# Optimization experiments

Hardware: AMD Instinct MI355X
Metric: run time of the kernel (lower is better)

Reference implementation:

```python
import jax, jax.numpy as jnp
import numpy as np

WINDOW_SIZE = 11
VAL_RANGE = 1.0
N_CHANNEL = 3
MS_WEIGHTS = jnp.array([0.0448, 0.2856, 0.3001, 0.2363, 0.1333], dtype=jnp.float32)


def _gaussian_window(window_size, sigma, channel):
    x = jnp.arange(window_size, dtype=jnp.float32)
    g = jnp.exp(-((x - window_size // 2) ** 2) / (2.0 * sigma ** 2))
    g = g / jnp.sum(g)
    w2d = jnp.outer(g, g)  # [ws, ws]
    # depthwise kernel in OIHW with feature_group_count=channel: [C, 1, ws, ws]
    return jnp.broadcast_to(w2d[None, None], (channel, 1, window_size, window_size))


def _dwconv(x, kernel):
    # x: [B, C, H, W], kernel: [C, 1, ws, ws], valid padding, groups=C
    return jax.lax.conv_general_dilated(
        x, kernel, window_strides=(1, 1), padding='VALID',
        dimension_numbers=('NCHW', 'OIHW', 'NCHW'),
        feature_group_count=kernel.shape[0])


def _avg_pool2(x):
    # kernel 2, stride 2, no padding (floor mode)
    s = jax.lax.reduce_window(x, 0.0, jax.lax.add,
                              (1, 1, 2, 2), (1, 1, 2, 2), 'VALID')
    return s * 0.25


def setup_inputs() -> dict:
    key = jax.random.key(0)
    k1, k2 = jax.random.split(key)
    output = jax.random.uniform(k1, (16, 3, 512, 512), dtype=jnp.float32)
    target = jax.random.uniform(k2, (16, 3, 512, 512), dtype=jnp.float32)
    return {"output": output, "target": target}


def reference(output, target):
    window = _gaussian_window(WINDOW_SIZE, 1.5, N_CHANNEL)
    L = VAL_RANGE
    C1 = (0.01 * L) ** 2
    C2 = (0.03 * L) ** 2
    cs_list, ssim_list = [], []
    for _ in range(MS_WEIGHTS.shape[0]):
        mu1 = _dwconv(output, window)
        mu2 = _dwconv(target, window)
        sigma1_sq = _dwconv(output * output, window) - mu1 * mu1
        sigma2_sq = _dwconv(target * target, window) - mu2 * mu2
        sigma12 = _dwconv(output * target, window) - mu1 * mu2
        denom = sigma1_sq + sigma2_sq + C2
        cs = (2.0 * sigma12 + C2) / denom
        ssim = (2.0 * mu1 * mu2 + C1) * (2.0 * sigma12 + C2) / (
            (mu1 * mu1 + mu2 * mu2 + C1) * denom)
        cs_list.append(jax.nn.relu(jnp.mean(cs)))
        ssim_list.append(jax.nn.relu(jnp.mean(ssim)))
        output = _avg_pool2(output)
        target = _avg_pool2(target)
    cs = (jnp.stack(cs_list) + 1.0) / 2.0
    ssim = (jnp.stack(ssim_list) + 1.0) / 2.0
    ms_ssim = jnp.prod((cs ** MS_WEIGHTS)[:-1]) * (ssim ** MS_WEIGHTS)[-1]
    return 1.0 - ms_ssim
```

## Files before the change

kernel.cpp:

```cpp
#include <hip/hip_runtime.h>

#define HALO 10
#define NIMG 48

#define GWLIST { 0.0010284f, 0.0075987f, 0.0360008f, 0.1093607f, 0.2130056f, \
                 0.2660117f, 0.2130056f, 0.1093607f, 0.0360008f, 0.0075987f, 0.0010284f }

#define PP   48
#define PSZ  (48 * 48)
#define HT0  (5 * PSZ)
#define HTP  48
#define HTSZ (32 * 48)
#define LDSH (HT0 + 5 * HTSZ)

typedef _Float16 half8 __attribute__((ext_vector_type(8)));
typedef _Float16 half4 __attribute__((ext_vector_type(4)));
typedef float    floatx4 __attribute__((ext_vector_type(4)));

template <bool FUSE>
__global__ __launch_bounds__(256, 4) void ssim_mfma_kernel(
    const float* __restrict__ A, const float* __restrict__ B,
    int H, int W, float2* __restrict__ partial,
    float* __restrict__ poolA, float* __restrict__ poolB)
{
    __shared__ __align__(16) _Float16 sm[LDSH];
    __shared__ float red[16];

    const float w[11] = GWLIST;
    const int tid  = threadIdx.x;
    const int lane = tid & 63;
    const int wv   = tid >> 6;
    const int gx0  = blockIdx.x * 32;
    const int gy0  = blockIdx.y * 32;
    const int z    = blockIdx.z;
    const float* a = A + (size_t)z * H * W;
    const float* b = B + (size_t)z * H * W;

    half8 wfrag;
    {
        int base = ((lane >> 4) << 3) - (lane & 15);
        #pragma unroll
        for (int i = 0; i < 8; ++i) {
            int j = base + i;
            float v = 0.f;
            #pragma unroll
            for (int J = 0; J < 11; ++J) v = (j == J) ? w[J] : v;
            wfrag[i] = (_Float16)v;
        }
    }

    const bool fast = (gy0 + 48 <= H) && (gx0 + 48 <= W);
    for (int e = tid; e < 288; e += 256) {
        int r = e / 6, c8 = e - r * 6;
        float fa[8], fb[8];
        if (fast) {
            const float* pa = a + (size_t)(gy0 + r) * W + gx0 + c8 * 8;
            const float* pb = b + (size_t)(gy0 + r) * W + gx0 + c8 * 8;
            *(float4*)&fa[0] = *(const float4*)pa;
            *(float4*)&fa[4] = *(const float4*)(pa + 4);
            *(float4*)&fb[0] = *(const float4*)pb;
            *(float4*)&fb[4] = *(const float4*)(pb + 4);
        } else {
            int gy = gy0 + r;
            #pragma unroll
            for (int i = 0; i < 8; ++i) {
                int gx = gx0 + c8 * 8 + i;
                bool ok = (gy < H) && (gx < W);
                size_t idx = (size_t)gy * W + gx;
                fa[i] = ok ? a[idx] : 0.f;
                fb[i] = ok ? b[idx] : 0.f;
            }
        }
        half8 ha, hb, haa, hbb, hab;
        #pragma unroll
        for (int i = 0; i < 8; ++i) {
            ha[i] = (_Float16)fa[i];
            hb[i] = (_Float16)fb[i];
            float qa = (float)ha[i];
            float qb = (float)hb[i];
            haa[i] = (_Float16)(qa * qa);
            hbb[i] = (_Float16)(qb * qb);
            hab[i] = (_Float16)(qa * qb);
        }
        int o = r * PP + c8 * 8;
        *(half8*)&sm[o + 0 * PSZ] = ha;
        *(half8*)&sm[o + 1 * PSZ] = hb;
        *(half8*)&sm[o + 2 * PSZ] = haa;
        *(half8*)&sm[o + 3 * PSZ] = hbb;
        *(half8*)&sm[o + 4 * PSZ] = hab;
    }
    __syncthreads();

    {
        const int arow = (lane & 15) * PP + ((lane >> 4) << 3);
        const int crow = (lane & 15) * HTP + ((lane >> 4) << 2);
        for (int jj = wv; jj < 30; jj += 4) {
            int q = jj / 6, rem = jj - q * 6;
            int m0 = (rem >> 1) << 4;
            int x0 = (rem & 1) << 4;
            half8 afrag = *(const half8*)&sm[q * PSZ + m0 * PP + x0 + arow];
            floatx4 c = {0.f, 0.f, 0.f, 0.f};
            c = __builtin_amdgcn_mfma_f32_16x16x32_f16(afrag, wfrag, c, 0, 0, 0);
            half4 hv;
            hv[0] = (_Float16)c[0]; hv[1] = (_Float16)c[1];
            hv[2] = (_Float16)c[2]; hv[3] = (_Float16)c[3];
            *(half4*)&sm[HT0 + q * HTSZ + x0 * HTP + m0 + crow] = hv;
        }
    }
    __syncthreads();

    float csSum = 0.f, ssimSum = 0.f;
    {
        const int y0 = (wv >> 1) << 4;
        const int x0 = (wv & 1) << 4;
        const int brow = (lane & 15) * HTP + ((lane >> 4) << 3);
        floatx4 m[5];
        #pragma unroll
        for (int q = 0; q < 5; ++q) {
            half8 bfrag = *(const half8*)&sm[HT0 + q * HTSZ + x0 * HTP + y0 + brow];
            floatx4 c = {0.f, 0.f, 0.f, 0.f};
            m[q] = __builtin_amdgcn_mfma_f32_16x16x32_f16(wfrag, bfrag, c, 0, 0, 0);
        }
        const int OH = H - HALO, OW = W - HALO;
        const int gx  = gx0 + x0 + (lane & 15);
        const int gyb = gy0 + y0 + ((lane >> 4) << 2);
        const float C1 = 1e-4f;
        const float C2 = 9e-4f;
        if (gx < OW) {
            #pragma unroll
            for (int i = 0; i < 4; ++i) {
                int gy = gyb + i;
                if (gy < OH) {
                    float mu1 = m[0][i], mu2 = m[1][i];
                    float s1sq = m[2][i] - mu1 * mu1;
                    float s2sq = m[3][i] - mu2 * mu2;
                    float s12  = m[4][i] - mu1 * mu2;
                    float denom = s1sq + s2sq + C2;
                    float num   = 2.f * s12 + C2;
                    float csv = num * __frcp_rn(denom);
                    float ssv = csv * (2.f * mu1 * mu2 + C1) *
                                __frcp_rn(mu1 * mu1 + mu2 * mu2 + C1);
                    csSum   += csv;
                    ssimSum += ssv;
                }
            }
        }
    }

    #pragma unroll
    for (int off = 32; off > 0; off >>= 1) {
        csSum   += __shfl_down(csSum, off, 64);
        ssimSum += __shfl_down(ssimSum, off, 64);
    }
    if (lane == 0) {
        red[wv]     = csSum;
        red[8 + wv] = ssimSum;
    }
    __syncthreads();
    if (tid == 0) {
        float c = 0.f, s = 0.f;
        #pragma unroll
        for (int i = 0; i < 4; ++i) { c += red[i]; s += red[8 + i]; }
        int slot = (z * gridDim.y + blockIdx.y) * gridDim.x + blockIdx.x;
        partial[slot] = make_float2(c, s);
    }

    if (FUSE && tid < 128) {
        const int OH2 = H >> 1, OW2 = W >> 1;
        const int img = tid >> 6;
        const int rem = tid & 63;
        const int pr  = rem >> 2;
        const int pq  = rem & 3;
        const float* src = img ? b : a;
        float* dst = (img ? poolB : poolA) + (size_t)z * OH2 * OW2;
        size_t base = (size_t)(gy0 + 2 * pr) * W + gx0 + pq * 8;
        float4 r0 = *(const float4*)(src + base);
        float4 r1 = *(const float4*)(src + base + 4);
        float4 r2 = *(const float4*)(src + base + W);
        float4 r3 = *(const float4*)(src + base + W + 4);
        float4 o;
        o.x = 0.25f * (r0.x + r0.y + r2.x + r2.y);
        o.y = 0.25f * (r0.z + r0.w + r2.z + r2.w);
        o.z = 0.25f * (r1.x + r1.y + r3.x + r3.y);
        o.w = 0.25f * (r1.z + r1.w + r3.z + r3.w);
        *(float4*)(dst + (size_t)((gy0 >> 1) + pr) * OW2 + (gx0 >> 1) + pq * 4) = o;
    }
}

#define TH   32
#define ROWS (TH + HALO)
#define HSTR 32
#define HQ   (ROWS * HSTR)

template <bool FUSE>
__global__ __launch_bounds__(256, 5) void ssim_scalar_kernel(
    const float* __restrict__ A, const float* __restrict__ B,
    int H, int W, float2* __restrict__ partial,
    float* __restrict__ poolA, float* __restrict__ poolB)
{
    __shared__ __align__(16) float lds[5 * HQ];
    __shared__ float red[16];

    const float w[11] = GWLIST;

    const int tid = threadIdx.x;
    const int gx0 = blockIdx.x * 32;
    const int gy0 = blockIdx.y * TH;
    const int z   = blockIdx.z;
    const float* a = A + (size_t)z * H * W;
    const float* b = B + (size_t)z * H * W;

    const bool fast = (gy0 + ROWS <= H) && (gx0 + 44 <= W);
    for (int e = tid; e < ROWS * 8; e += 256) {
        int r = e >> 3, c0 = (e & 7) * 4;
        int gy = gy0 + r;
        float s1[4]  = {0.f, 0.f, 0.f, 0.f};
        float s2[4]  = {0.f, 0.f, 0.f, 0.f};
        float s11[4] = {0.f, 0.f, 0.f, 0.f};
        float s22[4] = {0.f, 0.f, 0.f, 0.f};
        float s12[4] = {0.f, 0.f, 0.f, 0.f};
        #pragma unroll
        for (int c = 0; c < 4; ++c) {
            float ea[4], eb[4];
            if (fast) {
                const float* pa = a + (size_t)gy * W + gx0 + c0 + 4 * c;
                const float* pb = b + (size_t)gy * W + gx0 + c0 + 4 * c;
                *(float4*)&ea[0] = *(const float4*)pa;
                *(float4*)&eb[0] = *(const float4*)pb;
            } else {
                #pragma unroll
                for (int t = 0; t < 4; ++t) {
                    int gx = gx0 + c0 + 4 * c + t;
                    bool ok = (gy < H) && (gx < W);
                    size_t idx = (size_t)gy * W + gx;
                    ea[t] = ok ? a[idx] : 0.f;
                    eb[t] = ok ? b[idx] : 0.f;
                }
            }
            #pragma unroll
            for (int mm = 0; mm < 4; ++mm) {
                const int i = 4 * c + mm;
                float va = ea[mm], vb = eb[mm];
                float vaa = va * va, vbb = vb * vb, vab = va * vb;
                #pragma unroll
                for (int k = 0; k < 4; ++k) {
                    const int j = i - k;
                    if (j >= 0 && j <= 10) {
                        float wj = w[j];
                        s1[k]  += wj * va;
                        s2[k]  += wj * vb;
                        s11[k] += wj * vaa;
                        s22[k] += wj * vbb;
                        s12[k] += wj * vab;
                    }
                }
            }
        }
        int hb = r * HSTR + c0;
        *(float4*)&lds[hb + 0 * HQ] = make_float4(s1[0],  s1[1],  s1[2],  s1[3]);
        *(float4*)&lds[hb + 1 * HQ] = make_float4(s2[0],  s2[1],  s2[2],  s2[3]);
        *(float4*)&lds[hb + 2 * HQ] = make_float4(s11[0], s11[1], s11[2], s11[3]);
        *(float4*)&lds[hb + 3 * HQ] = make_float4(s22[0], s22[1], s22[2], s22[3]);
        *(float4*)&lds[hb + 4 * HQ] = make_float4(s12[0], s12[1], s12[2], s12[3]);
    }
    __syncthreads();

    const float C1 = 1e-4f;
    const float C2 = 9e-4f;
    float csSum = 0.f, ssimSum = 0.f;
    {
        const int ox  = tid & 31;
        const int oy0 = (tid >> 5) * 4;
        float m[5][4];
        #pragma unroll
        for (int q = 0; q < 5; ++q) {
            const float* hq = &lds[q * HQ + oy0 * HSTR + ox];
            float win[14];
            #pragma unroll
            for (int i = 0; i < 14; ++i) win[i] = hq[i * HSTR];
            #pragma unroll
            for (int k = 0; k < 4; ++k) {
                float acc = 0.f;
                #pragma unroll
                for (int j = 0; j < 11; ++j) acc += w[j] * win[k + j];
                m[q][k] = acc;
            }
        }
        const int OH = H - HALO, OW = W - HALO;
        const int gx = gx0 + ox;
        #pragma unroll
        for (int k = 0; k < 4; ++k) {
            int gy = gy0 + oy0 + k;
            if (gy < OH && gx < OW) {
                float mu1 = m[0][k], mu2 = m[1][k];
                float s1sq = m[2][k] - mu1 * mu1;
                float s2sq = m[3][k] - mu2 * mu2;
                float s12  = m[4][k] - mu1 * mu2;
                float denom  = s1sq + s2sq + C2;
                float num_cs = 2.f * s12 + C2;
                float csv = num_cs * __frcp_rn(denom);
                float ssv = csv * (2.f * mu1 * mu2 + C1) *
                            __frcp_rn(mu1 * mu1 + mu2 * mu2 + C1);
                csSum   += csv;
                ssimSum += ssv;
            }
        }
    }

    #pragma unroll
    for (int off = 32; off > 0; off >>= 1) {
        csSum   += __shfl_down(csSum, off, 64);
        ssimSum += __shfl_down(ssimSum, off, 64);
    }
    int wave = tid >> 6, lane = tid & 63;
    if (lane == 0) {
        red[wave]     = csSum;
        red[8 + wave] = ssimSum;
    }
    __syncthreads();
    if (tid == 0) {
        float c = 0.f, s = 0.f;
        #pragma unroll
        for (int i = 0; i < 4; ++i) { c += red[i]; s += red[8 + i]; }
        int slot = (z * gridDim.y + blockIdx.y) * gridDim.x + blockIdx.x;
        partial[slot] = make_float2(c, s);
    }

    if (FUSE && tid < 128) {
        const int OH2 = H >> 1, OW2 = W >> 1;
        const int img = tid >> 6;
        const int rem = tid & 63;
        const int pr  = rem >> 2;
        const int pq  = rem & 3;
        const float* src = img ? b : a;
        float* dst = (img ? poolB : poolA) + (size_t)z * OH2 * OW2;
        size_t base = (size_t)(gy0 + 2 * pr) * W + gx0 + pq * 8;
        float4 r0 = *(const float4*)(src + base);
        float4 r1 = *(const float4*)(src + base + 4);
        float4 r2 = *(const float4*)(src + base + W);
        float4 r3 = *(const float4*)(src + base + W + 4);
        float4 o;
        o.x = 0.25f * (r0.x + r0.y + r2.x + r2.y);
        o.y = 0.25f * (r0.z + r0.w + r2.z + r2.w);
        o.z = 0.25f * (r1.x + r1.y + r3.x + r3.y);
        o.w = 0.25f * (r1.z + r1.w + r3.z + r3.w);
        *(float4*)(dst + (size_t)((gy0 >> 1) + pr) * OW2 + (gx0 >> 1) + pq * 4) = o;
    }
}

__global__ void final_kernel(const float2* __restrict__ partial, float* __restrict__ out) {
    __shared__ double red[8];
    __shared__ double resC[5], resS[5];
    const int segs[6] = {0, 12288, 15360, 16128, 16320, 16368};
    const int tid = threadIdx.x;
    for (int s = 0; s < 5; ++s) {
        double c = 0.0, v = 0.0;
        for (int i = segs[s] + tid; i < segs[s + 1]; i += 256) {
            float2 p = partial[i];
            c += (double)p.x;
            v += (double)p.y;
        }
        #pragma unroll
        for (int off = 32; off > 0; off >>= 1) {
            c += __shfl_down(c, off, 64);
            v += __shfl_down(v, off, 64);
        }
        int wave = tid >> 6, lane = tid & 63;
        __syncthreads();
        if (lane == 0) { red[wave] = c; red[4 + wave] = v; }
        __syncthreads();
        if (tid == 0) {
            resC[s] = red[0] + red[1] + red[2] + red[3];
            resS[s] = red[4] + red[5] + red[6] + red[7];
        }
    }
    __syncthreads();
    if (tid == 0) {
        const double wgt[5] = {0.0448, 0.2856, 0.3001, 0.2363, 0.1333};
        double ms = 1.0;
        for (int s = 0; s < 5; ++s) {
            int Hs = 512 >> s;
            double cnt = (double)NIMG * (double)(Hs - 10) * (double)(Hs - 10);
            double cs = resC[s] / cnt;
            double sv = resS[s] / cnt;
            if (cs < 0.0) cs = 0.0;
            if (sv < 0.0) sv = 0.0;
            cs = (cs + 1.0) * 0.5;
            sv = (sv + 1.0) * 0.5;
            ms *= pow((s < 4) ? cs : sv, wgt[s]);
        }
        out[0] = (float)(1.0 - ms);
    }
}

extern "C" void kernel_launch(void* const* d_in, const int* in_sizes, int n_in,
                              void* d_out, int out_size, void* d_ws, size_t ws_size,
                              hipStream_t stream) {
    (void)in_sizes; (void)n_in; (void)out_size; (void)ws_size;
    const float* A0 = (const float*)d_in[0];
    const float* B0 = (const float*)d_in[1];
    float* out = (float*)d_out;

    char* ws = (char*)d_ws;
    float2* partial = (float2*)ws;
    float* pyr = (float*)(ws + (1 << 18));

    float* pa[5] = {nullptr, nullptr, nullptr, nullptr, nullptr};
    float* pb[5] = {nullptr, nullptr, nullptr, nullptr, nullptr};
    size_t off = 0;
    for (int s = 1; s <= 4; ++s) {
        int Hs = 512 >> s;
        size_t n = (size_t)NIMG * Hs * Hs;
        pa[s] = pyr + off; off += n;
        pb[s] = pyr + off; off += n;
    }

    const int segs[5] = {0, 12288, 15360, 16128, 16320};

    const float* curA = A0;
    const float* curB = B0;
    for (int s = 0; s < 5; ++s) {
        int Hs = 512 >> s;
        int g  = Hs >> 5;
        dim3 grid(g, g, NIMG);
        if (s < 2) {
            ssim_mfma_kernel<true><<<grid, 256, 0, stream>>>(
                curA, curB, Hs, Hs, partial + segs[s], pa[s + 1], pb[s + 1]);
            curA = pa[s + 1];
            curB = pb[s + 1];
        } else if (s < 4) {
            ssim_scalar_kernel<true><<<grid, 256, 0, stream>>>(
                curA, curB, Hs, Hs, partial + segs[s], pa[s + 1], pb[s + 1]);
            curA = pa[s + 1];
            curB = pb[s + 1];
        } else {
            ssim_scalar_kernel<false><<<grid, 256, 0, stream>>>(
                curA, curB, Hs, Hs, partial + segs[s], nullptr, nullptr);
        }
    }

    final_kernel<<<1, 256, 0, stream>>>(partial, out);
}
```

Measured before the change: 242.8 us.

## Alias horizontal-pass buffer onto input tiles, pad LDS rows, raise occupancy

The horizontal-pass results are now held in registers and written back into the same LDS region that held the input planes, behind an extra barrier. This removes the separate horizontal-transpose buffer and shrinks shared memory so that launch bounds can ask for 5 blocks per CU. Row pitch is padded from 48 to 56 halves to reduce LDS bank conflicts. The weight fragment is built once by the first wave and read from LDS, the products are computed as packed half vectors, and the final reduction loop is unrolled. The costs are an extra barrier, more register pressure from holding the results, and a different fp16 rounding for the squared terms.

```diff
diff --git a/kernel.cpp b/kernel.cpp
--- a/kernel.cpp
+++ b/kernel.cpp
@@ -6,19 +6,19 @@
 #define GWLIST { 0.0010284f, 0.0075987f, 0.0360008f, 0.1093607f, 0.2130056f, \
                  0.2660117f, 0.2130056f, 0.1093607f, 0.0360008f, 0.0075987f, 0.0010284f }
 
-#define PP   48
-#define PSZ  (48 * 48)
-#define HT0  (5 * PSZ)
-#define HTP  48
-#define HTSZ (32 * 48)
-#define LDSH (HT0 + 5 * HTSZ)
+#define PP   56
+#define PSZ  (48 * 56)
+#define HTP  56
+#define HTSZ (32 * 56)
+#define WT0  (5 * PSZ)
+#define LDSH (WT0 + 64 * 8)
 
 typedef _Float16 half8 __attribute__((ext_vector_type(8)));
 typedef _Float16 half4 __attribute__((ext_vector_type(4)));
 typedef float    floatx4 __attribute__((ext_vector_type(4)));
 
 template <bool FUSE>
-__global__ __launch_bounds__(256, 4) void ssim_mfma_kernel(
+__global__ __launch_bounds__(256, 5) void ssim_mfma_kernel(
     const float* __restrict__ A, const float* __restrict__ B,
     int H, int W, float2* __restrict__ partial,
     float* __restrict__ poolA, float* __restrict__ poolB)
@@ -36,17 +36,18 @@
     const float* a = A + (size_t)z * H * W;
     const float* b = B + (size_t)z * H * W;
 
-    half8 wfrag;
-    {
-        int base = ((lane >> 4) << 3) - (lane & 15);
+    if (tid < 64) {
+        int base = ((tid >> 4) << 3) - (tid & 15);
+        half8 wf;
         #pragma unroll
         for (int i = 0; i < 8; ++i) {
             int j = base + i;
             float v = 0.f;
             #pragma unroll
             for (int J = 0; J < 11; ++J) v = (j == J) ? w[J] : v;
-            wfrag[i] = (_Float16)v;
-        }
+            wf[i] = (_Float16)v;
+        }
+        *(half8*)&sm[WT0 + tid * 8] = wf;
     }
 
     const bool fast = (gy0 + 48 <= H) && (gx0 + 48 <= W);
@@ -71,17 +72,15 @@
                 fb[i] = ok ? b[idx] : 0.f;
             }
         }
-        half8 ha, hb, haa, hbb, hab;
+        half8 ha, hb;
         #pragma unroll
         for (int i = 0; i < 8; ++i) {
             ha[i] = (_Float16)fa[i];
             hb[i] = (_Float16)fb[i];
-            float qa = (float)ha[i];
-            float qb = (float)hb[i];
-            haa[i] = (_Float16)(qa * qa);
-            hbb[i] = (_Float16)(qb * qb);
-            hab[i] = (_Float16)(qa * qb);
-        }
+        }
+        half8 haa = ha * ha;
+        half8 hbb = hb * hb;
+        half8 hab = ha * hb;
         int o = r * PP + c8 * 8;
         *(half8*)&sm[o + 0 * PSZ] = ha;
         *(half8*)&sm[o + 1 * PSZ] = hb;
@@ -91,20 +90,41 @@
     }
     __syncthreads();
 
+    const half8 wfrag = *(const half8*)&sm[WT0 + lane * 8];
+
+    half4 res[8];
     {
         const int arow = (lane & 15) * PP + ((lane >> 4) << 3);
+        #pragma unroll
+        for (int u = 0; u < 8; ++u) {
+            int jj = wv + 4 * u;
+            if (jj < 30) {
+                int q = jj / 6, rem = jj - q * 6;
+                int m0 = (rem >> 1) << 4;
+                int x0 = (rem & 1) << 4;
+                half8 afrag = *(const half8*)&sm[q * PSZ + m0 * PP + x0 + arow];
+                floatx4 c = {0.f, 0.f, 0.f, 0.f};
+                c = __builtin_amdgcn_mfma_f32_16x16x32_f16(afrag, wfrag, c, 0, 0, 0);
+                half4 hv;
+                hv[0] = (_Float16)c[0]; hv[1] = (_Float16)c[1];
+                hv[2] = (_Float16)c[2]; hv[3] = (_Float16)c[3];
+                res[u] = hv;
+            }
+        }
+    }
+    __syncthreads();
+
+    {
         const int crow = (lane & 15) * HTP + ((lane >> 4) << 2);
-        for (int jj = wv; jj < 30; jj += 4) {
-            int q = jj / 6, rem = jj - q * 6;
-            int m0 = (rem >> 1) << 4;
-            int x0 = (rem & 1) << 4;
-            half8 afrag = *(const half8*)&sm[q * PSZ + m0 * PP + x0 + arow];
-            floatx4 c = {0.f, 0.f, 0.f, 0.f};
-            c = __builtin_amdgcn_mfma_f32_16x16x32_f16(afrag, wfrag, c, 0, 0, 0);
-            half4 hv;
-            hv[0] = (_Float16)c[0]; hv[1] = (_Float16)c[1];
-            hv[2] = (_Float16)c[2]; hv[3] = (_Float16)c[3];
-            *(half4*)&sm[HT0 + q * HTSZ + x0 * HTP + m0 + crow] = hv;
+        #pragma unroll
+        for (int u = 0; u < 8; ++u) {
+            int jj = wv + 4 * u;
+            if (jj < 30) {
+                int q = jj / 6, rem = jj - q * 6;
+                int m0 = (rem >> 1) << 4;
+                int x0 = (rem & 1) << 4;
+                *(half4*)&sm[q * HTSZ + x0 * HTP + m0 + crow] = res[u];
+            }
         }
     }
     __syncthreads();
@@ -117,7 +137,7 @@
         floatx4 m[5];
         #pragma unroll
         for (int q = 0; q < 5; ++q) {
-            half8 bfrag = *(const half8*)&sm[HT0 + q * HTSZ + x0 * HTP + y0 + brow];
+            half8 bfrag = *(const half8*)&sm[q * HTSZ + x0 * HTP + y0 + brow];
             floatx4 c = {0.f, 0.f, 0.f, 0.f};
             m[q] = __builtin_amdgcn_mfma_f32_16x16x32_f16(wfrag, bfrag, c, 0, 0, 0);
         }
@@ -355,6 +375,7 @@
     const int tid = threadIdx.x;
     for (int s = 0; s < 5; ++s) {
         double c = 0.0, v = 0.0;
+        #pragma unroll 4
         for (int i = segs[s] + tid; i < segs[s + 1]; i += 256) {
             float2 p = partial[i];
             c += (double)p.x;
```

New measurement: 214.8 us. 1.13x faster.
